# Performance work log

Measured on AMD Instinct MI355X. Metric: run time of the kernel, lower is better.

Reference implementation:

```python
import jax, jax.numpy as jnp
import numpy as np

B, D, H = 32768, 1024, 16
HD = D // H  # head_dim = 64
EPS = 1e-5


def setup_inputs() -> dict:
    key = jax.random.key(0)
    ks = jax.random.split(key, 12)
    s = 1.0 / np.sqrt(D)
    return {
        "sa_hidden": jax.random.normal(ks[0], (B, D), jnp.float32),
        "state_hidden": jax.random.normal(ks[1], (B, D), jnp.float32),
        "Wq": jax.random.normal(ks[2], (D, D), jnp.float32) * s,
        "bq": jax.random.normal(ks[3], (D,), jnp.float32) * s,
        "Wk": jax.random.normal(ks[4], (D, D), jnp.float32) * s,
        "bk": jax.random.normal(ks[5], (D,), jnp.float32) * s,
        "Wv": jax.random.normal(ks[6], (D, D), jnp.float32) * s,
        "bv": jax.random.normal(ks[7], (D,), jnp.float32) * s,
        "Wo": jax.random.normal(ks[8], (D, D), jnp.float32) * s,
        "bo": jax.random.normal(ks[9], (D,), jnp.float32) * s,
        "ln_w": jnp.ones((D,), jnp.float32),
        "ln_b": jnp.zeros((D,), jnp.float32),
    }


def reference(sa_hidden, state_hidden, Wq, bq, Wk, bk, Wv, bv, Wo, bo, ln_w, ln_b):
    b = sa_hidden.shape[0]
    # QKV projections (torch Linear: x @ W.T + b)
    Q = (sa_hidden @ Wq.T + bq).reshape(b, H, HD)
    K = (state_hidden @ Wk.T + bk).reshape(b, H, HD)
    V = (state_hidden @ Wv.T + bv).reshape(b, H, HD)
    # head-wise attention: [b, H, H] scores over the heads axis
    energy = jnp.einsum("bhd,bgd->bhg", Q, K) / np.sqrt(HD).astype(np.float32)
    attn = jax.nn.softmax(energy, axis=-1)
    out = jnp.einsum("bhg,bgd->bhd", attn, V)  # [b, H, HD]
    # transpose(1,2).view(b, D): flatten in (head_dim, heads) order
    out = jnp.swapaxes(out, 1, 2).reshape(b, D)
    out = out @ Wo.T + bo
    # residual + LayerNorm
    x = out + sa_hidden
    mu = jnp.mean(x, axis=-1, keepdims=True)
    var = jnp.mean((x - mu) ** 2, axis=-1, keepdims=True)
    return (x - mu) * jax.lax.rsqrt(var + EPS) * ln_w + ln_b
```

## Files before the change

### kernel.cpp

```cpp
#include <hip/hip_runtime.h>

typedef unsigned int  uint32;
typedef float  f32x4   __attribute__((ext_vector_type(4)));
typedef __bf16 bf16x8  __attribute__((ext_vector_type(8)));
typedef short  s16x4   __attribute__((ext_vector_type(4)));

__device__ __forceinline__ float bf2f(unsigned int u) {
  return __builtin_bit_cast(float, u << 16);
}
__device__ __forceinline__ unsigned short f2bf(float f) {
  uint32 u = __builtin_bit_cast(uint32, f);
  u += 0x7fffu + ((u >> 16) & 1u);
  return (unsigned short)(u >> 16);
}

__device__ __forceinline__ void gload_lds16(const void* g, void* l) {
  __builtin_amdgcn_global_load_lds(
      (const __attribute__((address_space(1))) void*)g,
      (__attribute__((address_space(3))) void*)l, 16, 0, 0);
}

__global__ __launch_bounds__(256) void cast_kernel(
    const float* __restrict__ x, unsigned short* __restrict__ y, int n8) {
  int i = blockIdx.x * 256 + threadIdx.x;
  if (i >= n8) return;
  const float4* xp = (const float4*)x;
  float4 a = xp[2 * i], b = xp[2 * i + 1];
  uint4 o;
  o.x = (uint32)f2bf(a.x) | ((uint32)f2bf(a.y) << 16);
  o.y = (uint32)f2bf(a.z) | ((uint32)f2bf(a.w) << 16);
  o.z = (uint32)f2bf(b.x) | ((uint32)f2bf(b.y) << 16);
  o.w = (uint32)f2bf(b.z) | ((uint32)f2bf(b.w) << 16);
  ((uint4*)y)[i] = o;
}

__global__ __launch_bounds__(256) void cat2_kernel(
    const float* __restrict__ a, const float* __restrict__ b,
    float* __restrict__ o) {
  int i = blockIdx.x * 256 + threadIdx.x;
  o[i] = (i < 1024) ? a[i] : b[i - 1024];
}

template <int EPI>
__global__ __launch_bounds__(512, 2) void gemm256(
    const unsigned short* __restrict__ A, const unsigned short* __restrict__ W,
    const float* __restrict__ bias, const float* __restrict__ resid,
    unsigned short* __restrict__ Ob, float* __restrict__ Of,
    int M, int N, int K) {
  __shared__ char smem[131072];
  const int tid  = threadIdx.x;
  const int lane = tid & 63;
  const int wave = tid >> 6;
  const int wr   = wave >> 2;
  const int wc   = wave & 3;

  const int nwg = gridDim.x;
  const int xcd = blockIdx.x & 7;
  const int r   = blockIdx.x >> 3;
  const int NT  = N >> 8;
  const int m0  = (xcd * ((nwg >> 3) / NT) + r / NT) << 8;
  const int n0  = (r % NT) << 8;

  f32x4 acc[8][4];
#pragma unroll
  for (int m = 0; m < 8; ++m)
#pragma unroll
    for (int n = 0; n < 4; ++n) acc[m][n] = (f32x4)0.0f;

  const int pr8 = lane >> 3;
  const int cl  = (lane & 7) ^ pr8;
  const unsigned short* As = A + (size_t)(m0 + wave * 8 + pr8) * K + cl * 8;
  const unsigned short* Bs = W + (size_t)(n0 + wave * 8 + pr8) * K + cl * 8;
  const int dst = wave * 1024 + lane * 16;

#define STAGE(d, kt)                                                          \
  {                                                                           \
    char* sb = smem + (d) * 65536;                                            \
    const int ko = (kt) * 64;                                                 \
    _Pragma("unroll") for (int j = 0; j < 4; ++j)                             \
        gload_lds16(As + (size_t)(j * 64) * K + ko, sb + j * 8192 + dst);     \
    _Pragma("unroll") for (int j = 0; j < 4; ++j)                             \
        gload_lds16(Bs + (size_t)(j * 64) * K + ko,                           \
                    sb + 32768 + j * 8192 + dst);                             \
  }

  const int fr = lane & 15, kg = lane >> 4;
  int cA[2];
#pragma unroll
  for (int ks = 0; ks < 2; ++ks)
    cA[ks] = fr * 128 + (((ks * 4 + kg) ^ (fr & 7)) * 16);
  const int abase = wr * 16384;
  const int bbase = 32768 + wc * 8192;

#define PH_AB(base_, av_, bv_, mlo, ks)                                       \
  {                                                                           \
    _Pragma("unroll") for (int m = 0; m < 4; ++m)                             \
        av_[m] = *(const bf16x8*)((base_) + abase + ((mlo) + m) * 2048 +      \
                                  cA[ks]);                                    \
    _Pragma("unroll") for (int n = 0; n < 4; ++n)                             \
        bv_[n] = *(const bf16x8*)((base_) + bbase + n * 2048 + cA[ks]);       \
  }
#define PH_A(base_, av_, mlo, ks)                                             \
  {                                                                           \
    _Pragma("unroll") for (int m = 0; m < 4; ++m)                             \
        av_[m] = *(const bf16x8*)((base_) + abase + ((mlo) + m) * 2048 +      \
                                  cA[ks]);                                    \
  }
#define PH_MFMA(av_, bv_, mlo)                                                \
  __builtin_amdgcn_s_setprio(1);                                              \
  _Pragma("unroll") for (int m = 0; m < 4; ++m)                               \
      _Pragma("unroll") for (int n = 0; n < 4; ++n)                           \
          acc[(mlo) + m][n] = __builtin_amdgcn_mfma_f32_16x16x32_bf16(        \
              av_[m], bv_[n], acc[(mlo) + m][n], 0, 0, 0);                    \
  __builtin_amdgcn_s_setprio(0);

  const int nt = K >> 6;
  STAGE(0, 0);
  STAGE(1, 1);

  for (int t = 0; t < nt - 2; ++t) {
    asm volatile("s_waitcnt vmcnt(8)" ::: "memory");
    __builtin_amdgcn_s_barrier();
    const char* base = smem + (t & 1) * 65536;
    bf16x8 a0[4], a1[4], b0[4], b1[4];
    PH_AB(base, a0, b0, 0, 0);
    PH_MFMA(a0, b0, 0);
    PH_A(base, a1, 4, 0);
    PH_MFMA(a1, b0, 4);
    PH_AB(base, a0, b1, 0, 1);
    PH_MFMA(a0, b1, 0);
    PH_A(base, a1, 4, 1);
    asm volatile("s_waitcnt lgkmcnt(0)" ::: "memory");
    __builtin_amdgcn_s_barrier();
    STAGE(t & 1, t + 2);
    __builtin_amdgcn_sched_barrier(0);
    PH_MFMA(a1, b1, 4);
  }
#pragma unroll
  for (int tt = 0; tt < 2; ++tt) {
    if (tt == 0)
      asm volatile("s_waitcnt vmcnt(8)" ::: "memory");
    else
      asm volatile("s_waitcnt vmcnt(0)" ::: "memory");
    __builtin_amdgcn_s_barrier();
    const char* base = smem + ((nt - 2 + tt) & 1) * 65536;
    bf16x8 a0[4], a1[4], b0[4], b1[4];
    PH_AB(base, a0, b0, 0, 0);
    PH_MFMA(a0, b0, 0);
    PH_A(base, a1, 4, 0);
    PH_MFMA(a1, b0, 4);
    PH_AB(base, a0, b1, 0, 1);
    PH_MFMA(a0, b1, 0);
    PH_A(base, a1, 4, 1);
    PH_MFMA(a1, b1, 4);
  }

  const int r4 = (lane >> 4) * 4;
  float bvv[4];
#pragma unroll
  for (int n = 0; n < 4; ++n) bvv[n] = bias[n0 + wc * 64 + n * 16 + fr];
#pragma unroll
  for (int m = 0; m < 8; ++m) {
    const int rowb = m0 + wr * 128 + m * 16 + r4;
#pragma unroll
    for (int i = 0; i < 4; ++i) {
      const size_t rb = (size_t)(rowb + i) * N;
#pragma unroll
      for (int n = 0; n < 4; ++n) {
        const size_t idx = rb + (n0 + wc * 64 + n * 16 + fr);
        float v = acc[m][n][i] + bvv[n];
        if constexpr (EPI == 0) {
          Ob[idx] = f2bf(v);
        } else {
          Of[idx] = v + resid[idx];
        }
      }
    }
  }
#undef STAGE
#undef PH_AB
#undef PH_A
#undef PH_MFMA
}

__global__ __launch_bounds__(256) void attn_kernel(
    const unsigned short* __restrict__ Q, const unsigned short* __restrict__ KV,
    unsigned short* __restrict__ O) {
  const int tid  = threadIdx.x;
  const int lane = tid & 63;
  const int wave = tid >> 6;
  const int b    = blockIdx.x * 4 + wave;
  const size_t qb  = (size_t)b * 1024;
  const size_t kvb = (size_t)b * 2048;
  const int fr = lane & 15, kg = lane >> 4;

  const bf16x8 kf0 = *(const bf16x8*)(KV + kvb + fr * 64 + kg * 8);
  const bf16x8 kf1 = *(const bf16x8*)(KV + kvb + fr * 64 + 32 + kg * 8);
  const bf16x8 qf0 = *(const bf16x8*)(Q + qb + fr * 64 + kg * 8);
  const bf16x8 qf1 = *(const bf16x8*)(Q + qb + fr * 64 + 32 + kg * 8);

  s16x4 vb[4];
#pragma unroll
  for (int c = 0; c < 4; ++c) {
    const unsigned short* vp = KV + kvb + 1024 + c * 16 + fr + kg * 4 * 64;
    s16x4 t;
    t[0] = (short)vp[0];
    t[1] = (short)vp[64];
    t[2] = (short)vp[128];
    t[3] = (short)vp[192];
    vb[c] = t;
  }

  f32x4 es = (f32x4)0.0f;
  es = __builtin_amdgcn_mfma_f32_16x16x32_bf16(kf0, qf0, es, 0, 0, 0);
  es = __builtin_amdgcn_mfma_f32_16x16x32_bf16(kf1, qf1, es, 0, 0, 0);

  float s0 = es[0] * 0.125f, s1 = es[1] * 0.125f;
  float s2 = es[2] * 0.125f, s3 = es[3] * 0.125f;
  float mx = fmaxf(fmaxf(s0, s1), fmaxf(s2, s3));
  mx = fmaxf(mx, __shfl_xor(mx, 16, 64));
  mx = fmaxf(mx, __shfl_xor(mx, 32, 64));
  float e0 = __expf(s0 - mx), e1 = __expf(s1 - mx);
  float e2 = __expf(s2 - mx), e3 = __expf(s3 - mx);
  float sum = e0 + e1 + e2 + e3;
  sum += __shfl_xor(sum, 16, 64);
  sum += __shfl_xor(sum, 32, 64);
  const float inv = 1.0f / sum;

  s16x4 pa;
  pa[0] = (short)f2bf(e0 * inv);
  pa[1] = (short)f2bf(e1 * inv);
  pa[2] = (short)f2bf(e2 * inv);
  pa[3] = (short)f2bf(e3 * inv);

  unsigned short* Ob = O + qb;
#pragma unroll
  for (int c = 0; c < 4; ++c) {
    f32x4 o = __builtin_amdgcn_mfma_f32_16x16x16bf16_1k(pa, vb[c],
                                                        (f32x4)0.0f, 0, 0, 0);
    uint2 st;
    st.x = (uint32)f2bf(o[0]) | ((uint32)f2bf(o[1]) << 16);
    st.y = (uint32)f2bf(o[2]) | ((uint32)f2bf(o[3]) << 16);
    *(uint2*)(Ob + c * 256 + fr * 16 + kg * 4) = st;
  }
}

__global__ __launch_bounds__(256) void ln_kernel(
    float* __restrict__ Y, const float* __restrict__ gw,
    const float* __restrict__ gb) {
  float* y = Y + (size_t)blockIdx.x * 1024;
  const int tid = threadIdx.x;
  float4 v = ((const float4*)y)[tid];
  float s  = v.x + v.y + v.z + v.w;
  float s2 = v.x * v.x + v.y * v.y + v.z * v.z + v.w * v.w;
#pragma unroll
  for (int o = 32; o > 0; o >>= 1) {
    s  += __shfl_xor(s, o, 64);
    s2 += __shfl_xor(s2, o, 64);
  }
  __shared__ float rs[4], rq[4];
  const int wave = tid >> 6;
  if ((tid & 63) == 0) { rs[wave] = s; rq[wave] = s2; }
  __syncthreads();
  s  = rs[0] + rs[1] + rs[2] + rs[3];
  s2 = rq[0] + rq[1] + rq[2] + rq[3];
  const float mean = s * (1.f / 1024.f);
  const float var  = s2 * (1.f / 1024.f) - mean * mean;
  const float r = rsqrtf(var + 1e-5f);
  const float4 w = ((const float4*)gw)[tid];
  const float4 bb = ((const float4*)gb)[tid];
  float4 o;
  o.x = (v.x - mean) * r * w.x + bb.x;
  o.y = (v.y - mean) * r * w.y + bb.y;
  o.z = (v.z - mean) * r * w.z + bb.z;
  o.w = (v.w - mean) * r * w.w + bb.w;
  ((float4*)y)[tid] = o;
}

extern "C" void kernel_launch(void* const* d_in, const int* in_sizes, int n_in,
                              void* d_out, int out_size, void* d_ws,
                              size_t ws_size, hipStream_t stream) {
  const float* sa = (const float*)d_in[0];
  const float* st = (const float*)d_in[1];
  const float* Wq = (const float*)d_in[2];
  const float* bq = (const float*)d_in[3];
  const float* Wk = (const float*)d_in[4];
  const float* bk = (const float*)d_in[5];
  const float* Wv = (const float*)d_in[6];
  const float* bv = (const float*)d_in[7];
  const float* Wo = (const float*)d_in[8];
  const float* bo = (const float*)d_in[9];
  const float* lw = (const float*)d_in[10];
  const float* lb = (const float*)d_in[11];
  float* out = (float*)d_out;

  const int M = 32768, D = 1024;
  const size_t MiB = 1024 * 1024;
  char* w = (char*)d_ws;
  unsigned short* saB  = (unsigned short*)(w);
  unsigned short* stB  = (unsigned short*)(w + 64 * MiB);
  unsigned short* WqB  = (unsigned short*)(w + 128 * MiB);
  unsigned short* WkvB = (unsigned short*)(w + 130 * MiB);
  unsigned short* WoB  = (unsigned short*)(w + 134 * MiB);
  unsigned short* Qb   = (unsigned short*)(w + 136 * MiB);
  float* bkv = (float*)(w + 128 * MiB);
  unsigned short* KVb = (unsigned short*)d_out;
  unsigned short* attb = saB;

  const int nH8 = M * D / 8;
  const int nW8 = D * D / 8;
  cast_kernel<<<nH8 / 256, 256, 0, stream>>>(sa, saB, nH8);
  cast_kernel<<<nH8 / 256, 256, 0, stream>>>(st, stB, nH8);
  cast_kernel<<<nW8 / 256, 256, 0, stream>>>(Wq, WqB, nW8);
  cast_kernel<<<nW8 / 256, 256, 0, stream>>>(Wk, (unsigned short*)WkvB, nW8);
  cast_kernel<<<nW8 / 256, 256, 0, stream>>>(Wv, (unsigned short*)WkvB + D * D, nW8);
  cast_kernel<<<nW8 / 256, 256, 0, stream>>>(Wo, WoB, nW8);

  gemm256<0><<<(M / 256) * (D / 256), 512, 0, stream>>>(
      saB, WqB, bq, nullptr, Qb, nullptr, M, D, D);

  cat2_kernel<<<8, 256, 0, stream>>>(bk, bv, bkv);
  gemm256<0><<<(M / 256) * (2 * D / 256), 512, 0, stream>>>(
      stB, WkvB, bkv, nullptr, KVb, nullptr, M, 2 * D, D);

  attn_kernel<<<M / 4, 256, 0, stream>>>(Qb, KVb, attb);

  gemm256<1><<<(M / 256) * (D / 256), 512, 0, stream>>>(
      attb, WoB, bo, sa, nullptr, out, M, D, D);

  ln_kernel<<<M, 256, 0, stream>>>(out, lw, lb);
}
```

Before: 501.6 us.

## Restructure GEMM main loop to prefetch next tile first with per-phase barriers

The bf16 GEMM main loop now issues the global-to-LDS load for tile t+1 at the start of each iteration, instead of loading tile t+2 mid-iteration after the LDS reads. The separate two-iteration epilogue loop is gone. Each LDS-read/MFMA phase is now bracketed by workgroup barriers and an explicit lgkmcnt wait, so the waves run in lockstep. The aim is to overlap global loads with a whole tile of compute and to schedule LDS reads against MFMAs more cleanly. The cost is many more barriers per K-tile, which can stall waves and reduce latency hiding across the workgroup.

```diff
diff --git a/kernel.cpp b/kernel.cpp
--- a/kernel.cpp
+++ b/kernel.cpp
@@ -92,20 +92,13 @@
   const int abase = wr * 16384;
   const int bbase = 32768 + wc * 8192;
 
-#define PH_AB(base_, av_, bv_, mlo, ks)                                       \
-  {                                                                           \
-    _Pragma("unroll") for (int m = 0; m < 4; ++m)                             \
-        av_[m] = *(const bf16x8*)((base_) + abase + ((mlo) + m) * 2048 +      \
-                                  cA[ks]);                                    \
-    _Pragma("unroll") for (int n = 0; n < 4; ++n)                             \
-        bv_[n] = *(const bf16x8*)((base_) + bbase + n * 2048 + cA[ks]);       \
-  }
-#define PH_A(base_, av_, mlo, ks)                                             \
-  {                                                                           \
-    _Pragma("unroll") for (int m = 0; m < 4; ++m)                             \
-        av_[m] = *(const bf16x8*)((base_) + abase + ((mlo) + m) * 2048 +      \
-                                  cA[ks]);                                    \
-  }
+#define PH_A4(base_, av_, mlo, ks)                                            \
+  _Pragma("unroll") for (int m = 0; m < 4; ++m)                               \
+      av_[m] = *(const bf16x8*)((base_) + abase + ((mlo) + m) * 2048 +        \
+                                cA[ks]);
+#define PH_B4(base_, bv_, ks)                                                 \
+  _Pragma("unroll") for (int n = 0; n < 4; ++n)                               \
+      bv_[n] = *(const bf16x8*)((base_) + bbase + n * 2048 + cA[ks]);
 #define PH_MFMA(av_, bv_, mlo)                                                \
   __builtin_amdgcn_s_setprio(1);                                              \
   _Pragma("unroll") for (int m = 0; m < 4; ++m)                               \
@@ -116,43 +109,44 @@
 
   const int nt = K >> 6;
   STAGE(0, 0);
-  STAGE(1, 1);
-
-  for (int t = 0; t < nt - 2; ++t) {
-    asm volatile("s_waitcnt vmcnt(8)" ::: "memory");
-    __builtin_amdgcn_s_barrier();
+
+  for (int t = 0; t < nt; ++t) {
+    if (t + 1 < nt) {
+      STAGE((t + 1) & 1, t + 1);
+      asm volatile("s_waitcnt vmcnt(8)" ::: "memory");
+    } else {
+      asm volatile("s_waitcnt vmcnt(0)" ::: "memory");
+    }
+    __builtin_amdgcn_s_barrier();
+
     const char* base = smem + (t & 1) * 65536;
     bf16x8 a0[4], a1[4], b0[4], b1[4];
-    PH_AB(base, a0, b0, 0, 0);
+
+    PH_A4(base, a0, 0, 0);
+    PH_B4(base, b0, 0);
+    __builtin_amdgcn_s_barrier();
+    asm volatile("s_waitcnt lgkmcnt(0)" ::: "memory");
     PH_MFMA(a0, b0, 0);
-    PH_A(base, a1, 4, 0);
+    __builtin_amdgcn_s_barrier();
+
+    PH_A4(base, a1, 4, 0);
+    __builtin_amdgcn_s_barrier();
+    asm volatile("s_waitcnt lgkmcnt(0)" ::: "memory");
     PH_MFMA(a1, b0, 4);
-    PH_AB(base, a0, b1, 0, 1);
+    __builtin_amdgcn_s_barrier();
+
+    PH_A4(base, a0, 0, 1);
+    PH_B4(base, b1, 1);
+    __builtin_amdgcn_s_barrier();
+    asm volatile("s_waitcnt lgkmcnt(0)" ::: "memory");
     PH_MFMA(a0, b1, 0);
-    PH_A(base, a1, 4, 1);
+    __builtin_amdgcn_s_barrier();
+
+    PH_A4(base, a1, 4, 1);
+    __builtin_amdgcn_s_barrier();
     asm volatile("s_waitcnt lgkmcnt(0)" ::: "memory");
-    __builtin_amdgcn_s_barrier();
-    STAGE(t & 1, t + 2);
-    __builtin_amdgcn_sched_barrier(0);
     PH_MFMA(a1, b1, 4);
-  }
-#pragma unroll
-  for (int tt = 0; tt < 2; ++tt) {
-    if (tt == 0)
-      asm volatile("s_waitcnt vmcnt(8)" ::: "memory");
-    else
-      asm volatile("s_waitcnt vmcnt(0)" ::: "memory");
-    __builtin_amdgcn_s_barrier();
-    const char* base = smem + ((nt - 2 + tt) & 1) * 65536;
-    bf16x8 a0[4], a1[4], b0[4], b1[4];
-    PH_AB(base, a0, b0, 0, 0);
-    PH_MFMA(a0, b0, 0);
-    PH_A(base, a1, 4, 0);
-    PH_MFMA(a1, b0, 4);
-    PH_AB(base, a0, b1, 0, 1);
-    PH_MFMA(a0, b1, 0);
-    PH_A(base, a1, 4, 1);
-    PH_MFMA(a1, b1, 4);
+    __builtin_amdgcn_s_barrier();
   }
 
   const int r4 = (lane >> 4) * 4;
@@ -178,8 +172,8 @@
     }
   }
 #undef STAGE
-#undef PH_AB
-#undef PH_A
+#undef PH_A4
+#undef PH_B4
 #undef PH_MFMA
 }
 
```

Result: slower. 531.8 us (+6.0%).

## Merge cast launches, fuse Q and KV GEMMs, move residual add into LayerNorm

Applied to the files above, without the earlier changes.

The six cast launches become one prep kernel, and the separate bias-concat kernel is dropped by choosing between the k and v biases inside the GEMM epilogue. The Q and KV projection GEMMs run as one launch split by block index. The output GEMM now writes bf16 without the residual, and LayerNorm reads that bf16 result plus sa and applies the residual add itself. This cuts launch overhead, fills the GPU better for the projection GEMMs, and replaces the fp32 write and read-back of the output with bf16. The cost is an extra bf16 rounding of the output projection before the residual add, which lowers accuracy.

```diff
diff --git a/kernel.cpp b/kernel.cpp
--- a/kernel.cpp
+++ b/kernel.cpp
@@ -20,10 +20,8 @@
       (__attribute__((address_space(3))) void*)l, 16, 0, 0);
 }
 
-__global__ __launch_bounds__(256) void cast_kernel(
-    const float* __restrict__ x, unsigned short* __restrict__ y, int n8) {
-  int i = blockIdx.x * 256 + threadIdx.x;
-  if (i >= n8) return;
+__device__ __forceinline__ void cast8(const float* __restrict__ x,
+                                      unsigned short* __restrict__ y, int i) {
   const float4* xp = (const float4*)x;
   float4 a = xp[2 * i], b = xp[2 * i + 1];
   uint4 o;
@@ -34,29 +32,40 @@
   ((uint4*)y)[i] = o;
 }
 
-__global__ __launch_bounds__(256) void cat2_kernel(
-    const float* __restrict__ a, const float* __restrict__ b,
-    float* __restrict__ o) {
+__global__ __launch_bounds__(256) void prep_kernel(
+    const float* __restrict__ sa, const float* __restrict__ st,
+    const float* __restrict__ Wq, const float* __restrict__ Wk,
+    const float* __restrict__ Wv, const float* __restrict__ Wo,
+    unsigned short* __restrict__ saB, unsigned short* __restrict__ stB,
+    unsigned short* __restrict__ WqB, unsigned short* __restrict__ WkvB,
+    unsigned short* __restrict__ WoB, int nH8, int nW8) {
   int i = blockIdx.x * 256 + threadIdx.x;
-  o[i] = (i < 1024) ? a[i] : b[i - 1024];
-}
-
-template <int EPI>
-__global__ __launch_bounds__(512, 2) void gemm256(
+  if (i < nH8) { cast8(sa, saB, i); return; }
+  i -= nH8;
+  if (i < nH8) { cast8(st, stB, i); return; }
+  i -= nH8;
+  if (i < nW8) { cast8(Wq, WqB, i); return; }
+  i -= nW8;
+  if (i < nW8) { cast8(Wk, WkvB, i); return; }
+  i -= nW8;
+  if (i < nW8) { cast8(Wv, WkvB + (size_t)nW8 * 8, i); return; }
+  i -= nW8;
+  cast8(Wo, WoB, i);
+}
+
+__device__ __forceinline__ void gemm_body(
     const unsigned short* __restrict__ A, const unsigned short* __restrict__ W,
-    const float* __restrict__ bias, const float* __restrict__ resid,
-    unsigned short* __restrict__ Ob, float* __restrict__ Of,
-    int M, int N, int K) {
-  __shared__ char smem[131072];
+    const float* __restrict__ bias, const float* __restrict__ bias2,
+    unsigned short* __restrict__ Ob,
+    int M, int N, int K, int nwg, int bid, char* smem) {
   const int tid  = threadIdx.x;
   const int lane = tid & 63;
   const int wave = tid >> 6;
   const int wr   = wave >> 2;
   const int wc   = wave & 3;
 
-  const int nwg = gridDim.x;
-  const int xcd = blockIdx.x & 7;
-  const int r   = blockIdx.x >> 3;
+  const int xcd = bid & 7;
+  const int r   = bid >> 3;
   const int NT  = N >> 8;
   const int m0  = (xcd * ((nwg >> 3) / NT) + r / NT) << 8;
   const int n0  = (r % NT) << 8;
@@ -155,10 +164,11 @@
     PH_MFMA(a1, b1, 4);
   }
 
+  const float* bsel = (bias2 != nullptr && n0 >= 1024) ? (bias2 - 1024) : bias;
   const int r4 = (lane >> 4) * 4;
   float bvv[4];
 #pragma unroll
-  for (int n = 0; n < 4; ++n) bvv[n] = bias[n0 + wc * 64 + n * 16 + fr];
+  for (int n = 0; n < 4; ++n) bvv[n] = bsel[n0 + wc * 64 + n * 16 + fr];
 #pragma unroll
   for (int m = 0; m < 8; ++m) {
     const int rowb = m0 + wr * 128 + m * 16 + r4;
@@ -168,12 +178,7 @@
 #pragma unroll
       for (int n = 0; n < 4; ++n) {
         const size_t idx = rb + (n0 + wc * 64 + n * 16 + fr);
-        float v = acc[m][n][i] + bvv[n];
-        if constexpr (EPI == 0) {
-          Ob[idx] = f2bf(v);
-        } else {
-          Of[idx] = v + resid[idx];
-        }
+        Ob[idx] = f2bf(acc[m][n][i] + bvv[n]);
       }
     }
   }
@@ -181,6 +186,26 @@
 #undef PH_AB
 #undef PH_A
 #undef PH_MFMA
+}
+
+__global__ __launch_bounds__(512, 2) void gemm_qkv(
+    const unsigned short* A0, const unsigned short* W0, const float* b0,
+    unsigned short* C0, int N0, int nb0,
+    const unsigned short* A1, const unsigned short* W1, const float* b1lo,
+    const float* b1hi, unsigned short* C1, int N1, int M, int K) {
+  __shared__ char smem[131072];
+  if ((int)blockIdx.x < nb0)
+    gemm_body(A0, W0, b0, nullptr, C0, M, N0, K, nb0, blockIdx.x, smem);
+  else
+    gemm_body(A1, W1, b1lo, b1hi, C1, M, N1, K, gridDim.x - nb0,
+              blockIdx.x - nb0, smem);
+}
+
+__global__ __launch_bounds__(512, 2) void gemm_o(
+    const unsigned short* A, const unsigned short* W, const float* bias,
+    unsigned short* C, int M, int N, int K) {
+  __shared__ char smem[131072];
+  gemm_body(A, W, bias, nullptr, C, M, N, K, gridDim.x, blockIdx.x, smem);
 }
 
 __global__ __launch_bounds__(256) void attn_kernel(
@@ -245,12 +270,19 @@
   }
 }
 
-__global__ __launch_bounds__(256) void ln_kernel(
+__global__ __launch_bounds__(256) void ln2_kernel(
+    const unsigned short* __restrict__ Ob, const float* __restrict__ sa,
     float* __restrict__ Y, const float* __restrict__ gw,
     const float* __restrict__ gb) {
-  float* y = Y + (size_t)blockIdx.x * 1024;
+  const size_t rb = (size_t)blockIdx.x * 1024;
   const int tid = threadIdx.x;
-  float4 v = ((const float4*)y)[tid];
+  const uint2 ov = ((const uint2*)(Ob + rb))[tid];
+  const float4 sv = ((const float4*)(sa + rb))[tid];
+  float4 v;
+  v.x = bf2f(ov.x & 0xffff) + sv.x;
+  v.y = bf2f(ov.x >> 16) + sv.y;
+  v.z = bf2f(ov.y & 0xffff) + sv.z;
+  v.w = bf2f(ov.y >> 16) + sv.w;
   float s  = v.x + v.y + v.z + v.w;
   float s2 = v.x * v.x + v.y * v.y + v.z * v.z + v.w * v.w;
 #pragma unroll
@@ -274,7 +306,7 @@
   o.y = (v.y - mean) * r * w.y + bb.y;
   o.z = (v.z - mean) * r * w.z + bb.z;
   o.w = (v.w - mean) * r * w.w + bb.w;
-  ((float4*)y)[tid] = o;
+  ((float4*)(Y + rb))[tid] = o;
 }
 
 extern "C" void kernel_launch(void* const* d_in, const int* in_sizes, int n_in,
@@ -303,30 +335,24 @@
   unsigned short* WkvB = (unsigned short*)(w + 130 * MiB);
   unsigned short* WoB  = (unsigned short*)(w + 134 * MiB);
   unsigned short* Qb   = (unsigned short*)(w + 136 * MiB);
-  float* bkv = (float*)(w + 128 * MiB);
   unsigned short* KVb = (unsigned short*)d_out;
   unsigned short* attb = saB;
+  unsigned short* oB   = stB;
 
   const int nH8 = M * D / 8;
   const int nW8 = D * D / 8;
-  cast_kernel<<<nH8 / 256, 256, 0, stream>>>(sa, saB, nH8);
-  cast_kernel<<<nH8 / 256, 256, 0, stream>>>(st, stB, nH8);
-  cast_kernel<<<nW8 / 256, 256, 0, stream>>>(Wq, WqB, nW8);
-  cast_kernel<<<nW8 / 256, 256, 0, stream>>>(Wk, (unsigned short*)WkvB, nW8);
-  cast_kernel<<<nW8 / 256, 256, 0, stream>>>(Wv, (unsigned short*)WkvB + D * D, nW8);
-  cast_kernel<<<nW8 / 256, 256, 0, stream>>>(Wo, WoB, nW8);
-
-  gemm256<0><<<(M / 256) * (D / 256), 512, 0, stream>>>(
-      saB, WqB, bq, nullptr, Qb, nullptr, M, D, D);
-
-  cat2_kernel<<<8, 256, 0, stream>>>(bk, bv, bkv);
-  gemm256<0><<<(M / 256) * (2 * D / 256), 512, 0, stream>>>(
-      stB, WkvB, bkv, nullptr, KVb, nullptr, M, 2 * D, D);
+  prep_kernel<<<(2 * nH8 + 4 * nW8) / 256, 256, 0, stream>>>(
+      sa, st, Wq, Wk, Wv, Wo, saB, stB, WqB, WkvB, WoB, nH8, nW8);
+
+  const int nbQ  = (M / 256) * (D / 256);
+  const int nbKV = (M / 256) * (2 * D / 256);
+  gemm_qkv<<<nbQ + nbKV, 512, 0, stream>>>(
+      saB, WqB, bq, Qb, D, nbQ,
+      stB, WkvB, bk, bv, KVb, 2 * D, M, D);
 
   attn_kernel<<<M / 4, 256, 0, stream>>>(Qb, KVb, attb);
 
-  gemm256<1><<<(M / 256) * (D / 256), 512, 0, stream>>>(
-      attb, WoB, bo, sa, nullptr, out, M, D, D);
-
-  ln_kernel<<<M, 256, 0, stream>>>(out, lw, lb);
-}
+  gemm_o<<<nbQ, 512, 0, stream>>>(attb, WoB, bo, oB, M, D, D);
+
+  ln2_kernel<<<M, 256, 0, stream>>>(oB, sa, out, lw, lb);
+}
```

New measurement: 472.5 us. -5.8%, faster.
